# Kernel optimization log

Measured on AMD Instinct MI355X. Metric: run time of the kernel, lower is better.

Reference implementation:

```python
import jax, jax.numpy as jnp
import numpy as np

LEAKY_SLOPE = 0.2  # self.alpha


def setup_inputs() -> dict:
    key = jax.random.key(0)
    k1, k2, k3 = jax.random.split(key, 3)
    E, F, R = 512, 256, 4
    h = jax.random.normal(k1, (E, F), dtype=jnp.float32)
    adj = jax.random.uniform(k2, (R, E, E), dtype=jnp.float32)
    lin_w = jax.random.normal(k3, (F,), dtype=jnp.float32) * (1.0 / np.sqrt(F))
    lin_b = jnp.zeros((1,), dtype=jnp.float32)
    return {"h": h, "adj": adj, "lin_w": lin_w, "lin_b": lin_b}


def reference(h, adj, lin_w, lin_b):
    # h: [E, F], adj: [R, E, E]
    adj_agg = jax.nn.softmax(jnp.sum(adj, axis=0), axis=1)          # [E, E]
    # pairwise elementwise product: a_input[i, j] = h_i * h_j
    a_input = h[:, None, :] * h[None, :, :]                          # [E, E, F]
    attention = jax.nn.leaky_relu(adj_agg[:, :, None] * a_input,
                                  negative_slope=LEAKY_SLOPE)        # [E, E, F]
    attention = jax.nn.softmax(attention, axis=0)                    # softmax over i
    # dropout p=0.0 / eval mode -> identity
    # Linear(F -> 1): scores[i, j] = attention[i, j] . w + b
    scores = jnp.einsum('ijf,f->ij', attention, lin_w) + lin_b[0]    # [E, E]
    alpha = jax.nn.softmax(jnp.sum(scores, axis=0)[None, :, None], axis=1)  # [1, E, 1]
    # h_prime[i, f] = sum_j attention[i, j, f] * h[j, f]
    h_prime = jnp.einsum('ijf,jf->if', attention, h)                 # [E, F]
    return jax.nn.elu(h_prime), alpha
```

## Files before the change

### kernel.cpp

```cpp
#include <hip/hip_runtime.h>


#define EE 512
#define FF 256
#define RRR 4
#define LOG2E 1.44269504088896340736f
#define TT 8
#define NCH 8
#define CLEN 64

__global__ __launch_bounds__(256) void kA(const float* __restrict__ adj,
                                          float* __restrict__ s,
                                          float* __restrict__ Z,
                                          float* __restrict__ Hp,
                                          float* __restrict__ out) {
    const int i = blockIdx.x;
    const int t = threadIdx.x;
    Z[i * 256 + t]  = 0.f;
    Hp[i * 256 + t] = 0.f;
    if (i == 0) {
        out[EE * FF + t]       = 1.0f / EE;
        out[EE * FF + 256 + t] = 1.0f / EE;
    }
    const float* base = adj + (size_t)i * EE;
    float t0 = 0.f, t1 = 0.f;
#pragma unroll
    for (int r = 0; r < RRR; ++r) {
        t0 += base[(size_t)r * EE * EE + t];
        t1 += base[(size_t)r * EE * EE + t + 256];
    }
    const float e0 = __expf(t0);
    const float e1 = __expf(t1);
    __shared__ float red[256];
    red[t] = e0 + e1;
    __syncthreads();
    for (int off = 128; off > 0; off >>= 1) {
        if (t < off) red[t] += red[t + off];
        __syncthreads();
    }
    const float inv = 1.0f / red[0];
    s[(size_t)i * EE + t]       = e0 * inv;
    s[(size_t)i * EE + t + 256] = e1 * inv;
}

__global__ __launch_bounds__(256) void kB(const float* __restrict__ h,
                                          const float* __restrict__ s,
                                          float* __restrict__ Z) {
    const int j0 = blockIdx.x * TT;
    const int c  = blockIdx.y;
    const int i0 = c * CLEN;
    const int f  = threadIdx.x;
    __shared__ float4 sl4[CLEN * 2];
    if (f < CLEN * 2) {
        sl4[f] = ((const float4*)(s + (size_t)(i0 + (f >> 1)) * EE + j0))[f & 1];
    }
    __syncthreads();
    float hj[TT], Zl[TT];
#pragma unroll
    for (int tj = 0; tj < TT; ++tj) {
        hj[tj] = h[(size_t)(j0 + tj) * FF + f] * LOG2E;
        Zl[tj] = 0.f;
    }
#pragma unroll 4
    for (int ii = 0; ii < CLEN; ++ii) {
        const float hif = h[(size_t)(i0 + ii) * FF + f];
        const float4 sa = sl4[ii * 2];
        const float4 sb = sl4[ii * 2 + 1];
        float sv[8] = {sa.x, sa.y, sa.z, sa.w, sb.x, sb.y, sb.z, sb.w};
#pragma unroll
        for (int tj = 0; tj < TT; ++tj) {
            const float y = sv[tj] * hif * hj[tj];
            const float z = fmaxf(y, 0.2f * y);
            Zl[tj] += __builtin_amdgcn_exp2f(z);
        }
    }
#pragma unroll
    for (int tj = 0; tj < TT; ++tj)
        atomicAdd(&Z[(size_t)(j0 + tj) * FF + f], Zl[tj]);
}

__global__ __launch_bounds__(256) void kC(const float* __restrict__ h,
                                          const float* __restrict__ s,
                                          const float* __restrict__ Z,
                                          float* __restrict__ Hp) {
    const int i0 = blockIdx.x * TT;
    const int c  = blockIdx.y;
    const int j0 = c * CLEN;
    const int f  = threadIdx.x;
    __shared__ float4 sl4[CLEN * 2];
    {
        __shared__ float slf[CLEN * TT];
        for (int idx = f; idx < CLEN * TT; idx += 256)
            slf[idx] = s[(size_t)(i0 + (idx & 7)) * EE + j0 + (idx >> 3)];
        __syncthreads();
        if (f < CLEN * 2) sl4[f] = ((const float4*)slf)[f];
    }
    __syncthreads();
    float hl[TT], acc[TT];
#pragma unroll
    for (int ti = 0; ti < TT; ++ti) {
        hl[ti] = h[(size_t)(i0 + ti) * FF + f] * LOG2E;
        acc[ti] = 0.f;
    }
#pragma unroll 4
    for (int jj = 0; jj < CLEN; ++jj) {
        const float hjf = h[(size_t)(j0 + jj) * FF + f];
        const float gj  = hjf * __builtin_amdgcn_rcpf(Z[(size_t)(j0 + jj) * FF + f]);
        const float4 sa = sl4[jj * 2];
        const float4 sb = sl4[jj * 2 + 1];
        float sv[8] = {sa.x, sa.y, sa.z, sa.w, sb.x, sb.y, sb.z, sb.w};
#pragma unroll
        for (int ti = 0; ti < TT; ++ti) {
            const float y = sv[ti] * hl[ti] * hjf;
            const float z = fmaxf(y, 0.2f * y);
            acc[ti] = fmaf(__builtin_amdgcn_exp2f(z), gj, acc[ti]);
        }
    }
#pragma unroll
    for (int ti = 0; ti < TT; ++ti)
        atomicAdd(&Hp[(size_t)(i0 + ti) * FF + f], acc[ti]);
}

__global__ __launch_bounds__(256) void kC2(const float* __restrict__ Hp,
                                           float* __restrict__ out) {
    const int i = blockIdx.x, f = threadIdx.x;
    const float a = Hp[i * 256 + f];
    out[i * 256 + f] = (a > 0.f) ? a : (__expf(a) - 1.0f);
}

extern "C" void kernel_launch(void* const* d_in, const int* in_sizes, int n_in,
                              void* d_out, int out_size, void* d_ws, size_t ws_size,
                              hipStream_t stream) {
    const float* h   = (const float*)d_in[0];
    const float* adj = (const float*)d_in[1];

    float* s  = (float*)d_ws;
    float* Z  = s + (size_t)EE * EE;
    float* Hp = Z + (size_t)EE * FF;
    float* out = (float*)d_out;

    kA <<<EE, 256, 0, stream>>>(adj, s, Z, Hp, out);
    kB <<<dim3(EE / TT, NCH), 256, 0, stream>>>(h, s, Z);
    kC <<<dim3(EE / TT, NCH), 256, 0, stream>>>(h, s, Z, Hp);
    kC2<<<EE, 256, 0, stream>>>(Hp, out);
}
```

Before: 44.80 us.

## Fuse ELU epilogue into kC via last-block counter, split chunks finer, preload h

Removes the separate ELU kernel: the last block for each row tile finishes the ELU itself, found with a per-tile atomic counter and thread fences. The chunk count doubles (CLEN 64 to 32), giving twice as many blocks for better occupancy. Each thread now preloads the chunk's h values and Z reciprocals into registers before the loop. The cost is more atomics on Z/Hp and higher register pressure.

```diff
diff --git a/kernel.cpp b/kernel.cpp
--- a/kernel.cpp
+++ b/kernel.cpp
@@ -6,14 +6,15 @@
 #define RRR 4
 #define LOG2E 1.44269504088896340736f
 #define TT 8
-#define NCH 8
-#define CLEN 64
+#define NCH 16
+#define CLEN 32
 
 __global__ __launch_bounds__(256) void kA(const float* __restrict__ adj,
                                           float* __restrict__ s,
                                           float* __restrict__ Z,
                                           float* __restrict__ Hp,
-                                          float* __restrict__ out) {
+                                          float* __restrict__ out,
+                                          int* __restrict__ cnt) {
     const int i = blockIdx.x;
     const int t = threadIdx.x;
     Z[i * 256 + t]  = 0.f;
@@ -21,6 +22,7 @@
     if (i == 0) {
         out[EE * FF + t]       = 1.0f / EE;
         out[EE * FF + 256 + t] = 1.0f / EE;
+        if (t < EE / TT) cnt[t] = 0;
     }
     const float* base = adj + (size_t)i * EE;
     float t0 = 0.f, t1 = 0.f;
@@ -47,14 +49,15 @@
                                           const float* __restrict__ s,
                                           float* __restrict__ Z) {
     const int j0 = blockIdx.x * TT;
-    const int c  = blockIdx.y;
-    const int i0 = c * CLEN;
+    const int i0 = blockIdx.y * CLEN;
     const int f  = threadIdx.x;
     __shared__ float4 sl4[CLEN * 2];
-    if (f < CLEN * 2) {
+    if (f < CLEN * 2)
         sl4[f] = ((const float4*)(s + (size_t)(i0 + (f >> 1)) * EE + j0))[f & 1];
-    }
     __syncthreads();
+    float hv[CLEN];
+#pragma unroll
+    for (int ii = 0; ii < CLEN; ++ii) hv[ii] = h[(size_t)(i0 + ii) * FF + f];
     float hj[TT], Zl[TT];
 #pragma unroll
     for (int tj = 0; tj < TT; ++tj) {
@@ -63,15 +66,13 @@
     }
 #pragma unroll 4
     for (int ii = 0; ii < CLEN; ++ii) {
-        const float hif = h[(size_t)(i0 + ii) * FF + f];
         const float4 sa = sl4[ii * 2];
         const float4 sb = sl4[ii * 2 + 1];
-        float sv[8] = {sa.x, sa.y, sa.z, sa.w, sb.x, sb.y, sb.z, sb.w};
+        const float sv[8] = {sa.x, sa.y, sa.z, sa.w, sb.x, sb.y, sb.z, sb.w};
 #pragma unroll
         for (int tj = 0; tj < TT; ++tj) {
-            const float y = sv[tj] * hif * hj[tj];
-            const float z = fmaxf(y, 0.2f * y);
-            Zl[tj] += __builtin_amdgcn_exp2f(z);
+            const float y = sv[tj] * hv[ii] * hj[tj];
+            Zl[tj] += __builtin_amdgcn_exp2f(fmaxf(y, 0.2f * y));
         }
     }
 #pragma unroll
@@ -82,20 +83,24 @@
 __global__ __launch_bounds__(256) void kC(const float* __restrict__ h,
                                           const float* __restrict__ s,
                                           const float* __restrict__ Z,
-                                          float* __restrict__ Hp) {
+                                          float* __restrict__ Hp,
+                                          float* __restrict__ out,
+                                          int* __restrict__ cnt) {
     const int i0 = blockIdx.x * TT;
-    const int c  = blockIdx.y;
-    const int j0 = c * CLEN;
+    const int j0 = blockIdx.y * CLEN;
     const int f  = threadIdx.x;
-    __shared__ float4 sl4[CLEN * 2];
+    __shared__ __align__(16) float slf[CLEN * TT];
     {
-        __shared__ float slf[CLEN * TT];
-        for (int idx = f; idx < CLEN * TT; idx += 256)
-            slf[idx] = s[(size_t)(i0 + (idx & 7)) * EE + j0 + (idx >> 3)];
-        __syncthreads();
-        if (f < CLEN * 2) sl4[f] = ((const float4*)slf)[f];
+        const int ti = f >> 5, jj = f & 31;
+        slf[jj * TT + ti] = s[(size_t)(i0 + ti) * EE + j0 + jj];
     }
     __syncthreads();
+    float hjv[CLEN], gj[CLEN];
+#pragma unroll
+    for (int jj = 0; jj < CLEN; ++jj) {
+        hjv[jj] = h[(size_t)(j0 + jj) * FF + f];
+        gj[jj]  = hjv[jj] * __builtin_amdgcn_rcpf(Z[(size_t)(j0 + jj) * FF + f]);
+    }
     float hl[TT], acc[TT];
 #pragma unroll
     for (int ti = 0; ti < TT; ++ti) {
@@ -104,28 +109,32 @@
     }
 #pragma unroll 4
     for (int jj = 0; jj < CLEN; ++jj) {
-        const float hjf = h[(size_t)(j0 + jj) * FF + f];
-        const float gj  = hjf * __builtin_amdgcn_rcpf(Z[(size_t)(j0 + jj) * FF + f]);
-        const float4 sa = sl4[jj * 2];
-        const float4 sb = sl4[jj * 2 + 1];
-        float sv[8] = {sa.x, sa.y, sa.z, sa.w, sb.x, sb.y, sb.z, sb.w};
+        const float4 sa = ((const float4*)slf)[jj * 2];
+        const float4 sb = ((const float4*)slf)[jj * 2 + 1];
+        const float sv[8] = {sa.x, sa.y, sa.z, sa.w, sb.x, sb.y, sb.z, sb.w};
 #pragma unroll
         for (int ti = 0; ti < TT; ++ti) {
-            const float y = sv[ti] * hl[ti] * hjf;
-            const float z = fmaxf(y, 0.2f * y);
-            acc[ti] = fmaf(__builtin_amdgcn_exp2f(z), gj, acc[ti]);
+            const float y = sv[ti] * hl[ti] * hjv[jj];
+            acc[ti] = fmaf(__builtin_amdgcn_exp2f(fmaxf(y, 0.2f * y)), gj[jj], acc[ti]);
         }
     }
 #pragma unroll
     for (int ti = 0; ti < TT; ++ti)
         atomicAdd(&Hp[(size_t)(i0 + ti) * FF + f], acc[ti]);
-}
 
-__global__ __launch_bounds__(256) void kC2(const float* __restrict__ Hp,
-                                           float* __restrict__ out) {
-    const int i = blockIdx.x, f = threadIdx.x;
-    const float a = Hp[i * 256 + f];
-    out[i * 256 + f] = (a > 0.f) ? a : (__expf(a) - 1.0f);
+    __threadfence();
+    __syncthreads();
+    __shared__ int sdone;
+    if (f == 0) sdone = (atomicAdd(&cnt[blockIdx.x], 1) == NCH - 1) ? 1 : 0;
+    __syncthreads();
+    if (sdone) {
+        __threadfence();
+#pragma unroll
+        for (int ti = 0; ti < TT; ++ti) {
+            const float a = Hp[(size_t)(i0 + ti) * FF + f];
+            out[(size_t)(i0 + ti) * FF + f] = (a > 0.f) ? a : (__expf(a) - 1.0f);
+        }
+    }
 }
 
 extern "C" void kernel_launch(void* const* d_in, const int* in_sizes, int n_in,
@@ -137,10 +146,10 @@
     float* s  = (float*)d_ws;
     float* Z  = s + (size_t)EE * EE;
     float* Hp = Z + (size_t)EE * FF;
+    int*  cnt = (int*)(Hp + (size_t)EE * FF);
     float* out = (float*)d_out;
 
-    kA <<<EE, 256, 0, stream>>>(adj, s, Z, Hp, out);
-    kB <<<dim3(EE / TT, NCH), 256, 0, stream>>>(h, s, Z);
-    kC <<<dim3(EE / TT, NCH), 256, 0, stream>>>(h, s, Z, Hp);
-    kC2<<<EE, 256, 0, stream>>>(Hp, out);
+    kA<<<EE, 256, 0, stream>>>(adj, s, Z, Hp, out, cnt);
+    kB<<<dim3(EE / TT, NCH), 256, 0, stream>>>(h, s, Z);
+    kC<<<dim3(EE / TT, NCH), 256, 0, stream>>>(h, s, Z, Hp, out, cnt);
 }
```

Result: slower. 95.71 us (+113.6%).
